# Optimization experiments

Hardware: AMD Instinct MI355X
Metric: run time of the kernel (lower is better)

The kernel has to match this reference:

```python
import jax, jax.numpy as jnp
import numpy as np

SEQ_LEN = 96      # input window length L
CHANNELS = 7      # enc_in C
FEAT_LEN = 7328   # L + L(L+1)/2 + sum_{i<L} sum_{i<=j<C} (L-j)
PRED_LEN = 720
BATCH = 256


def setup_inputs() -> dict:
    key = jax.random.key(0)
    k_x, k_w, k_b = jax.random.split(key, 3)
    x = jax.random.normal(k_x, (BATCH, SEQ_LEN, CHANNELS), dtype=jnp.float32)
    # nn.Linear(seq_len=7328, pred_len): W [out,in], b [out]
    bound = 1.0 / np.sqrt(FEAT_LEN)
    W = jax.random.uniform(k_w, (PRED_LEN, FEAT_LEN), dtype=jnp.float32, minval=-bound, maxval=bound)
    b = jax.random.uniform(k_b, (PRED_LEN,), dtype=jnp.float32, minval=-bound, maxval=bound)
    return {"x": x, "W": W, "b": b}


def _expand_features(x):
    # Faithful to: temp_2 = einsum('abd,acd->abcd', x, x); temp_3 = einsum('abce,ade->abcde', temp_2, x)
    # then concat of x, temp_2[:, i, i:] for i<L, and temp_3[:, i, j, j:] for i<L, i<=j<C
    # (range(i, C) is empty for i>=C, so only i<C contributes cubic terms).
    # We generate only the consumed triangular slices instead of the dense L^2/L^3 tensors.
    L = x.shape[1]
    C = x.shape[2]
    parts = [x]
    for i in range(L):
        # temp_2[:, i, i:] == x[:, i, :] * x[:, i:, :]   -> [B, L-i, C]
        parts.append(x[:, i:i + 1, :] * x[:, i:, :])
    for i in range(min(L, C)):
        for j in range(i, C):
            # temp_3[:, i, j, j:] == x[:, i] * x[:, j] * x[:, j:, :]  -> [B, L-j, C]
            parts.append(x[:, i:i + 1, :] * x[:, j:j + 1, :] * x[:, j:, :])
    return jnp.concatenate(parts, axis=1)  # [B, FEAT_LEN, C]


def reference(x, W, b):
    feat = _expand_features(x)                       # [B, 7328, C]
    # shared Linear applied along the feature/time axis (permute(0,2,1) -> Linear -> permute back)
    out = jnp.einsum('bsc,ps->bpc', feat, W) + b[None, :, None]  # [B, pred_len, C]
    return out
```

## Files before the change

kernel.cpp:

```cpp
#include <hip/hip_runtime.h>
#include <hip/hip_bf16.h>

#define L 96
#define CH 7
#define K_FEAT 7328
#define KPAD 7360
#define K8 (KPAD / 8)
#define KT64 115
#define Q_END 4752
#define PRED 720
#define NPAD 768
#define BATCH 256
#define M_TOT (BATCH * CH)
#define NSPLIT 6
#define W_BLKS (NPAD * K8 / 256)
#define TAB_BLKS ((K_FEAT + 255) / 256)

typedef __attribute__((ext_vector_type(8))) short bf16x8;
typedef __attribute__((ext_vector_type(4))) float f32x4;

#define SZ_A    ((size_t)M_TOT * KPAD * 2)
#define SZ_W    ((size_t)NPAD * KPAD * 2)
#define SZ_PS   ((size_t)NSPLIT * M_TOT * NPAD * 4)
#define OFF_AH  ((size_t)0)
#define OFF_WH  (OFF_AH + SZ_A)
#define OFF_PS  (OFF_WH + SZ_W)
#define OFF_TAB (OFF_PS + SZ_PS)
#define WS_REQ  (OFF_TAB + (size_t)K_FEAT * 8)

static __device__ __forceinline__ unsigned short f2bf(float f) {
    __hip_bfloat16 h = __float2bfloat16(f);
    return *(unsigned short*)&h;
}

static __device__ __forceinline__ void async_cp16(const unsigned short* g, unsigned short* l) {
    __builtin_amdgcn_global_load_lds(
        (const __attribute__((address_space(1))) unsigned int*)g,
        (__attribute__((address_space(3))) unsigned int*)l, 16, 0, 0);
}

static __device__ ushort4 feat_idx(int k) {
    unsigned short t1 = 96, t2 = 96, t3 = 0;
    if (k < L) {
        t3 = (unsigned short)k;
    } else if (k < Q_END) {
        int r = k - L;
        int i = 0, base = 0;
        while (base + (L - i) <= r) { base += L - i; ++i; }
        t2 = (unsigned short)i;
        t3 = (unsigned short)(i + (r - base));
    } else {
        int r = k - Q_END;
        int base = 0;
        for (int i = 0; i < CH; ++i) {
            for (int j = i; j < CH; ++j) {
                int len = L - j;
                if (r < base + len) {
                    return make_ushort4((unsigned short)i, (unsigned short)j,
                                        (unsigned short)(j + (r - base)), 0);
                }
                base += len;
            }
        }
    }
    return make_ushort4(t1, t2, t3, 0);
}

__global__ __launch_bounds__(256) void prep1(
    const float* __restrict__ W, unsigned short* __restrict__ Wh,
    ushort4* __restrict__ tab) {
    const int bid = blockIdx.x;
    const int tid = threadIdx.x;
    if (bid < W_BLKS) {
        int gid = bid * 256 + tid;
        int n = gid / K8, ch8 = gid - n * K8;
        int k = ch8 * 8;
        unsigned short o[8];
        #pragma unroll
        for (int j = 0; j < 8; ++j) {
            int kk = k + j;
            float v = (n < PRED && kk < K_FEAT) ? W[(size_t)n * K_FEAT + kk] : 0.0f;
            o[j] = f2bf(v);
        }
        *(uint4*)&Wh[(size_t)n * KPAD + k] = *(uint4*)o;
    } else {
        int k = (bid - W_BLKS) * 256 + tid;
        if (k < K_FEAT) tab[k] = feat_idx(k);
    }
}

__global__ __launch_bounds__(256) void featgen3(
    const float* __restrict__ x, const ushort4* __restrict__ tab,
    unsigned short* __restrict__ Ah) {
    __shared__ float xl[CH][L + 1];
    const int b = blockIdx.x >> 2;
    const int part = blockIdx.x & 3;
    const int tid = threadIdx.x;

    for (int i = tid; i < L * CH; i += 256) {
        int t = i / CH, c = i - t * CH;
        xl[c][t] = x[(size_t)b * L * CH + i];
    }
    if (tid < CH) xl[tid][L] = 1.0f;
    __syncthreads();

    const int span = CH * KPAD / 4;
    unsigned short* Ab = Ah + (size_t)b * CH * KPAD;
    const int e1 = (part + 1) * span;
    for (int e = part * span + tid; e < e1; e += 256) {
        int c = e / KPAD, kk = e - c * KPAD;
        float v = 0.0f;
        if (kk < K_FEAT) {
            ushort4 t = tab[kk];
            v = xl[c][t.x] * xl[c][t.y] * xl[c][t.z];
        }
        Ab[e] = f2bf(v);
    }
}

__global__ __launch_bounds__(256, 2) void gemm2(
    const unsigned short* __restrict__ Ah, const unsigned short* __restrict__ Wh,
    float* __restrict__ ps) {
    __shared__ unsigned short S[2][2][128 * 64];

    const int tid = threadIdx.x;
    const int lane = tid & 63;
    const int w = tid >> 6;
    const int wr = w >> 1, wc = w & 1;

    const int id = blockIdx.x;
    const int nid = (id & 7) * 63 + (id >> 3);
    const int bx = nid % 14;
    const int rest = nid / 14;
    const int by = rest % 6;
    const int bz = rest / 6;
    const int m0 = bx * 128;
    const int n0 = by * 128;
    const int kt0 = (KT64 * bz) / NSPLIT;
    const int kt1 = (KT64 * (bz + 1)) / NSPLIT;

    const int cg = (lane & 7) ^ (lane >> 3);
    const unsigned short* gA[4];
    const unsigned short* gW[4];
    #pragma unroll
    for (int q = 0; q < 4; ++q) {
        int row = w * 32 + q * 8 + (lane >> 3);
        gA[q] = Ah + (size_t)(m0 + row) * KPAD + cg * 8 + kt0 * 64;
        gW[q] = Wh + (size_t)(n0 + row) * KPAD + cg * 8 + kt0 * 64;
    }

#define STAGE(B) do { \
        _Pragma("unroll") \
        for (int q = 0; q < 4; ++q) { \
            async_cp16(gA[q], &S[B][0][(w * 256 + q * 64) * 8]); \
            async_cp16(gW[q], &S[B][1][(w * 256 + q * 64) * 8]); \
            gA[q] += 64; gW[q] += 64; \
        } \
    } while (0)

    const int lr = lane & 15;
    const int ck = lane >> 4;
    int offA[4][2], offW[4][2];
    #pragma unroll
    for (int mi = 0; mi < 4; ++mi) {
        int r = wr * 64 + mi * 16 + lr;
        #pragma unroll
        for (int h = 0; h < 2; ++h)
            offA[mi][h] = r * 128 + (((h * 4 + ck) ^ (r & 7)) << 4);
    }
    #pragma unroll
    for (int ni = 0; ni < 4; ++ni) {
        int r = wc * 64 + ni * 16 + lr;
        #pragma unroll
        for (int h = 0; h < 2; ++h)
            offW[ni][h] = r * 128 + (((h * 4 + ck) ^ (r & 7)) << 4);
    }

    f32x4 acc[4][4] = {};

    STAGE(0);
    __syncthreads();
    int cur = 0;
    for (int kt = kt0; kt < kt1; ++kt) {
        if (kt + 1 < kt1) STAGE(cur ^ 1);

        const char* baseA = (const char*)S[cur][0];
        const char* baseW = (const char*)S[cur][1];
        bf16x8 ah[4][2], wh[4][2];
        #pragma unroll
        for (int mi = 0; mi < 4; ++mi) {
            ah[mi][0] = *(const bf16x8*)(baseA + offA[mi][0]);
            ah[mi][1] = *(const bf16x8*)(baseA + offA[mi][1]);
        }
        #pragma unroll
        for (int ni = 0; ni < 4; ++ni) {
            wh[ni][0] = *(const bf16x8*)(baseW + offW[ni][0]);
            wh[ni][1] = *(const bf16x8*)(baseW + offW[ni][1]);
        }
        #pragma unroll
        for (int mi = 0; mi < 4; ++mi) {
            #pragma unroll
            for (int ni = 0; ni < 4; ++ni) {
                acc[mi][ni] = __builtin_amdgcn_mfma_f32_16x16x32_bf16(ah[mi][0], wh[ni][0], acc[mi][ni], 0, 0, 0);
                acc[mi][ni] = __builtin_amdgcn_mfma_f32_16x16x32_bf16(ah[mi][1], wh[ni][1], acc[mi][ni], 0, 0, 0);
            }
        }
        __syncthreads();
        cur ^= 1;
    }
#undef STAGE

    float* pb = ps + (size_t)bz * M_TOT * NPAD;
    #pragma unroll
    for (int mi = 0; mi < 4; ++mi) {
        #pragma unroll
        for (int ni = 0; ni < 4; ++ni) {
            const int n = n0 + wc * 64 + ni * 16 + lr;
            const int mr = m0 + wr * 64 + mi * 16 + ck * 4;
            #pragma unroll
            for (int r = 0; r < 4; ++r) {
                pb[(size_t)(mr + r) * NPAD + n] = acc[mi][ni][r];
            }
        }
    }
}

__global__ __launch_bounds__(256) void reduce_k(
    const float* __restrict__ ps, const float* __restrict__ bias,
    float* __restrict__ out) {
    int gid = blockIdx.x * 256 + threadIdx.x;
    int b = gid / PRED, p = gid - b * PRED;
    float bv = bias[p];
    float o[CH];
    #pragma unroll
    for (int c = 0; c < CH; ++c) o[c] = bv;
    #pragma unroll
    for (int s = 0; s < NSPLIT; ++s) {
        const float* pb = ps + (size_t)s * M_TOT * NPAD + (size_t)b * CH * NPAD + p;
        #pragma unroll
        for (int c = 0; c < CH; ++c) o[c] += pb[(size_t)c * NPAD];
    }
    float* ob = out + (size_t)gid * CH;
    #pragma unroll
    for (int c = 0; c < CH; ++c) ob[c] = o[c];
}

#define BM 64
#define BN 64
#define BK 32
#define XSTRIDE 101

__global__ void build_table(ushort4* __restrict__ tab) {
    int k = blockIdx.x * blockDim.x + threadIdx.x;
    if (k < K_FEAT) tab[k] = feat_idx(k);
}

__global__ __launch_bounds__(256) void fused_poly_gemm(
    const float* __restrict__ x, const float* __restrict__ W,
    const float* __restrict__ bias, const ushort4* __restrict__ tab,
    float* __restrict__ out) {
    __shared__ float xt[BM][XSTRIDE];
    __shared__ float At[BK][BM];
    __shared__ float Wt[BK][BN];

    const int tid = threadIdx.x;
    const int m0 = blockIdx.x * BM;
    const int n0 = blockIdx.y * BN;

    for (int idx = tid; idx < BM * L; idx += 256) {
        int r = idx / L, t = idx - r * L;
        int m = m0 + r;
        int b = m / CH, c = m - b * CH;
        xt[r][t] = x[(b * L + t) * CH + c];
    }
    if (tid < BM) xt[tid][96] = 1.0f;
    __syncthreads();

    const int tm = tid & 15;
    const int tn = tid >> 4;
    float acc[4][4] = {};

    for (int k0 = 0; k0 < K_FEAT; k0 += BK) {
        #pragma unroll
        for (int q = tid; q < 512; q += 256) {
            int n = q >> 3, kq = q & 7;
            float4 wv;
            if (n0 + n < PRED) wv = *(const float4*)&W[(size_t)(n0 + n) * K_FEAT + k0 + kq * 4];
            else wv = make_float4(0.f, 0.f, 0.f, 0.f);
            Wt[kq * 4 + 0][n] = wv.x; Wt[kq * 4 + 1][n] = wv.y;
            Wt[kq * 4 + 2][n] = wv.z; Wt[kq * 4 + 3][n] = wv.w;
        }
        {
            int k = tid >> 3, mg = tid & 7;
            ushort4 e = tab[k0 + k];
            float p[8];
            #pragma unroll
            for (int mm = 0; mm < 8; ++mm) {
                int m = mg * 8 + mm;
                p[mm] = xt[m][e.x] * xt[m][e.y] * xt[m][e.z];
            }
            *(float4*)&At[k][mg * 8]     = make_float4(p[0], p[1], p[2], p[3]);
            *(float4*)&At[k][mg * 8 + 4] = make_float4(p[4], p[5], p[6], p[7]);
        }
        __syncthreads();
        #pragma unroll 8
        for (int k = 0; k < BK; ++k) {
            float4 a = *(const float4*)&At[k][tm * 4];
            float4 wv = *(const float4*)&Wt[k][tn * 4];
            acc[0][0] = fmaf(a.x, wv.x, acc[0][0]); acc[0][1] = fmaf(a.x, wv.y, acc[0][1]);
            acc[0][2] = fmaf(a.x, wv.z, acc[0][2]); acc[0][3] = fmaf(a.x, wv.w, acc[0][3]);
            acc[1][0] = fmaf(a.y, wv.x, acc[1][0]); acc[1][1] = fmaf(a.y, wv.y, acc[1][1]);
            acc[1][2] = fmaf(a.y, wv.z, acc[1][2]); acc[1][3] = fmaf(a.y, wv.w, acc[1][3]);
            acc[2][0] = fmaf(a.z, wv.x, acc[2][0]); acc[2][1] = fmaf(a.z, wv.y, acc[2][1]);
            acc[2][2] = fmaf(a.z, wv.z, acc[2][2]); acc[2][3] = fmaf(a.z, wv.w, acc[2][3]);
            acc[3][0] = fmaf(a.w, wv.x, acc[3][0]); acc[3][1] = fmaf(a.w, wv.y, acc[3][1]);
            acc[3][2] = fmaf(a.w, wv.z, acc[3][2]); acc[3][3] = fmaf(a.w, wv.w, acc[3][3]);
        }
        __syncthreads();
    }
    #pragma unroll
    for (int i = 0; i < 4; ++i) {
        int m = m0 + tm * 4 + i;
        int b = m / CH, c = m - b * CH;
        #pragma unroll
        for (int j = 0; j < 4; ++j) {
            int n = n0 + tn * 4 + j;
            if (n < PRED) out[((size_t)b * PRED + n) * CH + c] = acc[i][j] + bias[n];
        }
    }
}

extern "C" void kernel_launch(void* const* d_in, const int* in_sizes, int n_in,
                              void* d_out, int out_size, void* d_ws, size_t ws_size,
                              hipStream_t stream) {
    const float* x    = (const float*)d_in[0];
    const float* W    = (const float*)d_in[1];
    const float* bias = (const float*)d_in[2];
    float* out = (float*)d_out;
    char* ws = (char*)d_ws;

    if (ws_size >= WS_REQ) {
        unsigned short* Ah = (unsigned short*)(ws + OFF_AH);
        unsigned short* Wh = (unsigned short*)(ws + OFF_WH);
        float* psum = (float*)(ws + OFF_PS);
        ushort4* tab = (ushort4*)(ws + OFF_TAB);

        hipLaunchKernelGGL(prep1, dim3(W_BLKS + TAB_BLKS), dim3(256), 0, stream, W, Wh, tab);
        hipLaunchKernelGGL(featgen3, dim3(BATCH * 4), dim3(256), 0, stream, x, tab, Ah);
        hipLaunchKernelGGL(gemm2, dim3(14 * 6 * NSPLIT), dim3(256), 0, stream, Ah, Wh, psum);
        hipLaunchKernelGGL(reduce_k, dim3(BATCH * PRED / 256), dim3(256), 0, stream,
                           psum, bias, out);
    } else {
        ushort4* tab = (ushort4*)ws;
        hipLaunchKernelGGL(build_table, dim3((K_FEAT + 255) / 256), dim3(256), 0, stream, tab);
        dim3 grid(M_TOT / BM, (PRED + BN - 1) / BN);
        hipLaunchKernelGGL(fused_poly_gemm, grid, dim3(256), 0, stream, x, W, bias, tab, out);
    }
}
```

Measured before the change: 76.45 us.

## Fuse split-K reduction into GEMM via atomic tickets and vectorize feature stores

The separate reduce kernel is removed. Each GEMM block now writes its partial tile, takes an atomic ticket on a per-tile counter, and the last of the NSPLIT blocks sums all partials, adds the bias and writes the output. The counters are zeroed by an extra block in the prep kernel. The feature-generation kernel now builds 8 bf16 values per thread and writes them as one 16-byte store instead of scalar 2-byte stores. This saves a kernel launch and the extra pass over the partial sums, at the cost of a serialized reduction tail in the last-arriving blocks and uncoalesced strided output writes.

```diff
diff --git a/kernel.cpp b/kernel.cpp
--- a/kernel.cpp
+++ b/kernel.cpp
@@ -13,6 +13,7 @@
 #define BATCH 256
 #define M_TOT (BATCH * CH)
 #define NSPLIT 6
+#define NTILE (14 * 6)
 #define W_BLKS (NPAD * K8 / 256)
 #define TAB_BLKS ((K_FEAT + 255) / 256)
 
@@ -26,7 +27,8 @@
 #define OFF_WH  (OFF_AH + SZ_A)
 #define OFF_PS  (OFF_WH + SZ_W)
 #define OFF_TAB (OFF_PS + SZ_PS)
-#define WS_REQ  (OFF_TAB + (size_t)K_FEAT * 8)
+#define OFF_CNT (OFF_TAB + (size_t)K_FEAT * 8)
+#define WS_REQ  (OFF_CNT + (size_t)NTILE * 4)
 
 static __device__ __forceinline__ unsigned short f2bf(float f) {
     __hip_bfloat16 h = __float2bfloat16(f);
@@ -68,7 +70,7 @@
 
 __global__ __launch_bounds__(256) void prep1(
     const float* __restrict__ W, unsigned short* __restrict__ Wh,
-    ushort4* __restrict__ tab) {
+    ushort4* __restrict__ tab, unsigned int* __restrict__ cnt) {
     const int bid = blockIdx.x;
     const int tid = threadIdx.x;
     if (bid < W_BLKS) {
@@ -83,13 +85,15 @@
             o[j] = f2bf(v);
         }
         *(uint4*)&Wh[(size_t)n * KPAD + k] = *(uint4*)o;
-    } else {
+    } else if (bid < W_BLKS + TAB_BLKS) {
         int k = (bid - W_BLKS) * 256 + tid;
         if (k < K_FEAT) tab[k] = feat_idx(k);
-    }
-}
-
-__global__ __launch_bounds__(256) void featgen3(
+    } else {
+        if (tid < NTILE) cnt[tid] = 0u;
+    }
+}
+
+__global__ __launch_bounds__(256) void featgen4(
     const float* __restrict__ x, const ushort4* __restrict__ tab,
     unsigned short* __restrict__ Ah) {
     __shared__ float xl[CH][L + 1];
@@ -104,24 +108,33 @@
     if (tid < CH) xl[tid][L] = 1.0f;
     __syncthreads();
 
-    const int span = CH * KPAD / 4;
+    const int span = CH * K8 / 4;
     unsigned short* Ab = Ah + (size_t)b * CH * KPAD;
-    const int e1 = (part + 1) * span;
-    for (int e = part * span + tid; e < e1; e += 256) {
-        int c = e / KPAD, kk = e - c * KPAD;
-        float v = 0.0f;
-        if (kk < K_FEAT) {
-            ushort4 t = tab[kk];
-            v = xl[c][t.x] * xl[c][t.y] * xl[c][t.z];
-        }
-        Ab[e] = f2bf(v);
-    }
-}
-
-__global__ __launch_bounds__(256, 2) void gemm2(
+    const int q1 = (part + 1) * span;
+    for (int q = part * span + tid; q < q1; q += 256) {
+        int c = q / K8, ch8 = q - c * K8;
+        int k = ch8 * 8;
+        unsigned short o[8];
+        #pragma unroll
+        for (int j = 0; j < 8; ++j) {
+            int kk = k + j;
+            float v = 0.0f;
+            if (kk < K_FEAT) {
+                ushort4 t = tab[kk];
+                v = xl[c][t.x] * xl[c][t.y] * xl[c][t.z];
+            }
+            o[j] = f2bf(v);
+        }
+        *(uint4*)&Ab[(size_t)c * KPAD + k] = *(uint4*)o;
+    }
+}
+
+__global__ __launch_bounds__(256, 2) void gemm3(
     const unsigned short* __restrict__ Ah, const unsigned short* __restrict__ Wh,
-    float* __restrict__ ps) {
+    const float* __restrict__ bias, float* __restrict__ ps,
+    unsigned int* __restrict__ cnt, float* __restrict__ out) {
     __shared__ unsigned short S[2][2][128 * 64];
+    __shared__ int ticket_s;
 
     const int tid = threadIdx.x;
     const int lane = tid & 63;
@@ -210,39 +223,53 @@
     }
 #undef STAGE
 
-    float* pb = ps + (size_t)bz * M_TOT * NPAD;
+    {
+        float* pb = ps + (size_t)bz * M_TOT * NPAD;
+        #pragma unroll
+        for (int mi = 0; mi < 4; ++mi) {
+            #pragma unroll
+            for (int ni = 0; ni < 4; ++ni) {
+                const int n = n0 + wc * 64 + ni * 16 + lr;
+                const int mr = m0 + wr * 64 + mi * 16 + ck * 4;
+                #pragma unroll
+                for (int r = 0; r < 4; ++r) {
+                    pb[(size_t)(mr + r) * NPAD + n] = acc[mi][ni][r];
+                }
+            }
+        }
+    }
+
+    __threadfence();
+    __syncthreads();
+    if (tid == 0) ticket_s = (int)atomicAdd(&cnt[bx * 6 + by], 1u);
+    __syncthreads();
+    if (ticket_s != NSPLIT - 1) return;
+    __threadfence();
+
     #pragma unroll
     for (int mi = 0; mi < 4; ++mi) {
         #pragma unroll
         for (int ni = 0; ni < 4; ++ni) {
             const int n = n0 + wc * 64 + ni * 16 + lr;
+            if (n >= PRED) continue;
             const int mr = m0 + wr * 64 + mi * 16 + ck * 4;
+            const float bv = bias[n];
+            float tot[4] = {bv, bv, bv, bv};
+            #pragma unroll
+            for (int s = 0; s < NSPLIT; ++s) {
+                const float* pb = ps + (size_t)s * M_TOT * NPAD + n;
+                #pragma unroll
+                for (int r = 0; r < 4; ++r)
+                    tot[r] += pb[(size_t)(mr + r) * NPAD];
+            }
             #pragma unroll
             for (int r = 0; r < 4; ++r) {
-                pb[(size_t)(mr + r) * NPAD + n] = acc[mi][ni][r];
-            }
-        }
-    }
-}
-
-__global__ __launch_bounds__(256) void reduce_k(
-    const float* __restrict__ ps, const float* __restrict__ bias,
-    float* __restrict__ out) {
-    int gid = blockIdx.x * 256 + threadIdx.x;
-    int b = gid / PRED, p = gid - b * PRED;
-    float bv = bias[p];
-    float o[CH];
-    #pragma unroll
-    for (int c = 0; c < CH; ++c) o[c] = bv;
-    #pragma unroll
-    for (int s = 0; s < NSPLIT; ++s) {
-        const float* pb = ps + (size_t)s * M_TOT * NPAD + (size_t)b * CH * NPAD + p;
-        #pragma unroll
-        for (int c = 0; c < CH; ++c) o[c] += pb[(size_t)c * NPAD];
-    }
-    float* ob = out + (size_t)gid * CH;
-    #pragma unroll
-    for (int c = 0; c < CH; ++c) ob[c] = o[c];
+                const int m = mr + r;
+                const int b = m / CH, c = m - b * CH;
+                out[((size_t)b * PRED + n) * CH + c] = tot[r];
+            }
+        }
+    }
 }
 
 #define BM 64
@@ -344,12 +371,13 @@
         unsigned short* Wh = (unsigned short*)(ws + OFF_WH);
         float* psum = (float*)(ws + OFF_PS);
         ushort4* tab = (ushort4*)(ws + OFF_TAB);
-
-        hipLaunchKernelGGL(prep1, dim3(W_BLKS + TAB_BLKS), dim3(256), 0, stream, W, Wh, tab);
-        hipLaunchKernelGGL(featgen3, dim3(BATCH * 4), dim3(256), 0, stream, x, tab, Ah);
-        hipLaunchKernelGGL(gemm2, dim3(14 * 6 * NSPLIT), dim3(256), 0, stream, Ah, Wh, psum);
-        hipLaunchKernelGGL(reduce_k, dim3(BATCH * PRED / 256), dim3(256), 0, stream,
-                           psum, bias, out);
+        unsigned int* cnt = (unsigned int*)(ws + OFF_CNT);
+
+        hipLaunchKernelGGL(prep1, dim3(W_BLKS + TAB_BLKS + 1), dim3(256), 0, stream,
+                           W, Wh, tab, cnt);
+        hipLaunchKernelGGL(featgen4, dim3(BATCH * 4), dim3(256), 0, stream, x, tab, Ah);
+        hipLaunchKernelGGL(gemm3, dim3(NTILE * NSPLIT), dim3(256), 0, stream,
+                           Ah, Wh, bias, psum, cnt, out);
     } else {
         ushort4* tab = (ushort4*)ws;
         hipLaunchKernelGGL(build_table, dim3((K_FEAT + 255) / 256), dim3(256), 0, stream, tab);
```

Measured after the change: 156.8 us. 105% more time.
